# Performance work log

Measured on AMD Instinct MI355X. Metric: run time of the kernel, lower is better.

The kernel has to match this reference:

```python
import jax, jax.numpy as jnp
import numpy as np

HEADS = 8
DIM = 512


def setup_inputs() -> dict:
    key = jax.random.key(0)
    ks = jax.random.split(key, 7)
    B, N, L, C = 2, 64, 32, DIM
    feat1 = jax.random.normal(ks[0], (B, N, L, C), dtype=jnp.float32)
    feat2 = jax.random.normal(ks[1], (B, N, L, C), dtype=jnp.float32)
    s = 1.0 / np.sqrt(C)
    Wq1 = jax.random.normal(ks[2], (C, C), dtype=jnp.float32) * s
    Wk1 = jax.random.normal(ks[3], (C, C), dtype=jnp.float32) * s
    Wq2 = jax.random.normal(ks[4], (C, C), dtype=jnp.float32) * s
    Wk2 = jax.random.normal(ks[5], (C, C), dtype=jnp.float32) * s
    tau = jnp.array(0.3, dtype=jnp.float32)
    return {"feat1": feat1, "feat2": feat2, "Wq1": Wq1, "Wk1": Wk1,
            "Wq2": Wq2, "Wk2": Wk2, "tau": tau}


def _proj_heads(x_flat, W, B, NL, H):
    # nn.Linear(bias=False): y = x @ W.T ; then split heads -> (B, H, NL, hd)
    y = jnp.einsum('btc,dc->btd', x_flat, W)
    return y.reshape(B, NL, H, -1).transpose(0, 2, 1, 3)


def _pooled_scores(Q, Kt, scale, tau, B, H, N, L):
    # scores (B,H,NL,NL) -> softmax -> view (B,H,N,L,N,L) -> amax(-1) -> mean(L) -> mean(H)
    s = jnp.einsum('bhqd,bhkd->bhqk', Q, Kt) * (scale / tau)
    s = jax.nn.softmax(s, axis=-1)
    s = s.reshape(B, H, N, L, N, L)
    s = s.max(axis=-1)          # (B,H,N,L,N)
    s = s.mean(axis=3)          # (B,H,N,N)
    return s.mean(axis=1)       # (B,N,N)


def reference(feat1, feat2, Wq1, Wk1, Wq2, Wk2, tau):
    B, N, L, C = feat1.shape
    H = HEADS
    NL = N * L
    scale = C ** (-0.5)
    f1 = feat1.reshape(B, NL, C)
    f2 = feat2.reshape(B, NL, C)
    Q1 = _proj_heads(f1, Wq1, B, NL, H)
    K1 = _proj_heads(f1, Wk1, B, NL, H)
    Q2 = _proj_heads(f2, Wq2, B, NL, H)
    K2 = _proj_heads(f2, Wk2, B, NL, H)
    c12 = _pooled_scores(Q1, K2, scale, tau, B, H, N, L)
    c21 = _pooled_scores(Q2, K1, scale, tau, B, H, N, L)
    return (c12 + c21) * 0.5
```

## Files before the change

kernel.cpp:

```cpp
#include <hip/hip_runtime.h>
#include <hip/hip_bf16.h>

#define NLQ 2048
#define CDIM 512
#define HD 64
#define NHEADS 8

typedef __attribute__((ext_vector_type(8))) short bf16x8;
typedef __attribute__((ext_vector_type(4))) float f32x4;

#define MFMA(A, B, Cc) __builtin_amdgcn_mfma_f32_16x16x32_bf16(A, B, Cc, 0, 0, 0)

__device__ __forceinline__ short f2bf(float x) {
    __hip_bfloat16 h = __float2bfloat16(x);
    return *reinterpret_cast<short*>(&h);
}

__device__ __forceinline__ float fast_exp2(float x) {
    float r;
    asm("v_exp_f32 %0, %1" : "=v"(r) : "v"(x));
    return r;
}

__device__ __forceinline__ int swz(int row, int colByte) {
    return ((row << 7) + colByte) ^ ((row & 7) << 4);
}

#define QK_ELEMS   8388608
#define X_ELEMS    2097152
#define W_ELEMS    262144
#define PLANE      2097152

__global__ __launch_bounds__(256) void convert_kernel(
    const float* __restrict__ f1, const float* __restrict__ f2,
    const float* __restrict__ Wq1, const float* __restrict__ Wk1,
    const float* __restrict__ Wq2, const float* __restrict__ Wk2,
    const float* __restrict__ tau, short* __restrict__ ws)
{
    short* Xb1 = ws + QK_ELEMS;
    short* Xb2 = Xb1 + X_ELEMS;
    short* Wb  = Xb2 + X_ELEMS;
    float la = 0.044194173824159216f * 1.4426950408889634f / tau[0];

    int bid = blockIdx.x;
    const float* src; short* dst; float a = 1.0f; int idx;
    if (bid < 1024)       { src = f1; dst = Xb1; idx = bid; }
    else if (bid < 2048)  { src = f2; dst = Xb2; idx = bid - 1024; }
    else {
        int wseg = (bid - 2048) >> 7;
        idx = (bid - 2048) & 127;
        src = (wseg == 0) ? Wq1 : (wseg == 1) ? Wk1 : (wseg == 2) ? Wq2 : Wk2;
        dst = Wb + wseg * W_ELEMS;
        a = (wseg == 0 || wseg == 2) ? la : 1.0f;
    }
    int off = idx * 2048 + threadIdx.x * 8;
    float4 x0 = *(const float4*)(src + off);
    float4 x1 = *(const float4*)(src + off + 4);
    bf16x8 v = { f2bf(x0.x * a), f2bf(x0.y * a), f2bf(x0.z * a), f2bf(x0.w * a),
                 f2bf(x1.x * a), f2bf(x1.y * a), f2bf(x1.z * a), f2bf(x1.w * a) };
    *(bf16x8*)(dst + off) = v;
}

__global__ __launch_bounds__(256) void proj_kernel(short* __restrict__ ws)
{
    int bid = blockIdx.x;
    int gx = bid >> 8;
    int mt = (bid >> 3) & 31;
    int nt = bid & 7;

    const short* X   = ws + QK_ELEMS + gx * X_ELEMS;
    const short* Wst = ws + QK_ELEMS + 2 * X_ELEMS + gx * (2 * W_ELEMS);
    short* Yb = ws;

    __shared__ alignas(16) short Alds[2][8192];
    __shared__ alignas(16) short Blds[2][8192];

    int t = threadIdx.x;
    int lane = t & 63;
    int w = t >> 6;
    int wr = w >> 1, wc = w & 1;
    int m0 = mt * 128, d0 = nt * 128;

    int srow = t >> 1;
    int sh = (t & 1) * 32;
    const short* xsrc = X   + (m0 + srow) * CDIM + sh;
    const short* wsrc = Wst + (d0 + srow) * CDIM + sh;

    f32x4 acc[4][4] = {};

    bf16x8 wv0 = *(const bf16x8*)(wsrc);
    bf16x8 wv1 = *(const bf16x8*)(wsrc + 8);
    bf16x8 wv2 = *(const bf16x8*)(wsrc + 16);
    bf16x8 wv3 = *(const bf16x8*)(wsrc + 24);
    bf16x8 xv0 = *(const bf16x8*)(xsrc);
    bf16x8 xv1 = *(const bf16x8*)(xsrc + 8);
    bf16x8 xv2 = *(const bf16x8*)(xsrc + 16);
    bf16x8 xv3 = *(const bf16x8*)(xsrc + 24);
    {
        int b0 = sh * 2;
        *(bf16x8*)((char*)Alds[0] + swz(srow, b0))      = wv0;
        *(bf16x8*)((char*)Alds[0] + swz(srow, b0 + 16)) = wv1;
        *(bf16x8*)((char*)Alds[0] + swz(srow, b0 + 32)) = wv2;
        *(bf16x8*)((char*)Alds[0] + swz(srow, b0 + 48)) = wv3;
        *(bf16x8*)((char*)Blds[0] + swz(srow, b0))      = xv0;
        *(bf16x8*)((char*)Blds[0] + swz(srow, b0 + 16)) = xv1;
        *(bf16x8*)((char*)Blds[0] + swz(srow, b0 + 32)) = xv2;
        *(bf16x8*)((char*)Blds[0] + swz(srow, b0 + 48)) = xv3;
    }
    __syncthreads();

    for (int kc = 0; kc < 8; ++kc) {
        int cur = kc & 1;
        if (kc < 7) {
            const short* xn = xsrc + (kc + 1) * 64;
            const short* wn = wsrc + (kc + 1) * 64;
            wv0 = *(const bf16x8*)(wn);      wv1 = *(const bf16x8*)(wn + 8);
            wv2 = *(const bf16x8*)(wn + 16); wv3 = *(const bf16x8*)(wn + 24);
            xv0 = *(const bf16x8*)(xn);      xv1 = *(const bf16x8*)(xn + 8);
            xv2 = *(const bf16x8*)(xn + 16); xv3 = *(const bf16x8*)(xn + 24);
        }
        int cb = (lane >> 4) << 4;
        bf16x8 bfr[4][2];
        #pragma unroll
        for (int ms = 0; ms < 4; ++ms) {
            int row = (wr << 6) + (ms << 4) + (lane & 15);
            bfr[ms][0] = *(const bf16x8*)((const char*)Blds[cur] + swz(row, cb));
            bfr[ms][1] = *(const bf16x8*)((const char*)Blds[cur] + swz(row, cb + 64));
        }
        #pragma unroll
        for (int ns = 0; ns < 4; ++ns) {
            int arow = (wc << 6) + (ns << 4) + (lane & 15);
            bf16x8 a0 = *(const bf16x8*)((const char*)Alds[cur] + swz(arow, cb));
            bf16x8 a1 = *(const bf16x8*)((const char*)Alds[cur] + swz(arow, cb + 64));
            #pragma unroll
            for (int ms = 0; ms < 4; ++ms) {
                acc[ms][ns] = MFMA(a0, bfr[ms][0], acc[ms][ns]);
                acc[ms][ns] = MFMA(a1, bfr[ms][1], acc[ms][ns]);
            }
        }
        if (kc < 7) {
            int nx = cur ^ 1;
            int b0 = sh * 2;
            *(bf16x8*)((char*)Alds[nx] + swz(srow, b0))      = wv0;
            *(bf16x8*)((char*)Alds[nx] + swz(srow, b0 + 16)) = wv1;
            *(bf16x8*)((char*)Alds[nx] + swz(srow, b0 + 32)) = wv2;
            *(bf16x8*)((char*)Alds[nx] + swz(srow, b0 + 48)) = wv3;
            *(bf16x8*)((char*)Blds[nx] + swz(srow, b0))      = xv0;
            *(bf16x8*)((char*)Blds[nx] + swz(srow, b0 + 16)) = xv1;
            *(bf16x8*)((char*)Blds[nx] + swz(srow, b0 + 32)) = xv2;
            *(bf16x8*)((char*)Blds[nx] + swz(srow, b0 + 48)) = xv3;
        }
        __syncthreads();
    }

    #pragma unroll
    for (int ms = 0; ms < 4; ++ms) {
        int m = m0 + (wr << 6) + (ms << 4) + (lane & 15);
        int bb = m >> 11, tl = m & 2047;
        #pragma unroll
        for (int ns = 0; ns < 4; ++ns) {
            int d = d0 + (wc << 6) + (ns << 4) + ((lane >> 4) << 2);
            int plane = (gx << 1) + (d >> 9);
            int head = (d >> 6) & 7;
            int hd = d & 63;
            short4 v = { f2bf(acc[ms][ns][0]), f2bf(acc[ms][ns][1]),
                         f2bf(acc[ms][ns][2]), f2bf(acc[ms][ns][3]) };
            *(short4*)(Yb + plane * PLANE + ((bb * NHEADS + head) * NLQ + tl) * HD + hd) = v;
        }
    }
}

__global__ __launch_bounds__(256) void attn_kernel(
    const short* __restrict__ qk, float* __restrict__ out)
{
    int bid = blockIdx.x;
    int combo = bid & 31;
    int qt = bid >> 5;
    int h    = combo & 7;
    int pair = (combo >> 3) & 1;
    int b    = combo >> 4;

    const short* Q = qk + (pair ? 2 : 0) * PLANE + (b * NHEADS + h) * NLQ * HD;
    const short* K = qk + (pair ? 1 : 3) * PLANE + (b * NHEADS + h) * NLQ * HD;

    __shared__ float bms[64][65];
    __shared__ float psums[4][64];
    __shared__ float rowinv[64];
    __shared__ float partial[4][64];

    int t = threadIdx.x;
    int lane = t & 63;
    int w = t >> 6;

    bf16x8 qb[4][2];
    #pragma unroll
    for (int qs = 0; qs < 4; ++qs) {
        int row = qt * 64 + (qs << 4) + (lane & 15);
        const short* qp = Q + row * HD + ((lane >> 4) << 3);
        qb[qs][0] = *(const bf16x8*)qp;
        qb[qs][1] = *(const bf16x8*)(qp + 32);
    }

    float ps[4] = {0.f, 0.f, 0.f, 0.f};

    for (int i = 0; i < 8; ++i) {
        int kt = (w << 3) + i;
        int k0 = kt << 6;

        bf16x8 af[4][2];
        #pragma unroll
        for (int ks = 0; ks < 4; ++ks) {
            const short* kp = K + (k0 + (ks << 4) + (lane & 15)) * HD + ((lane >> 4) << 3);
            af[ks][0] = *(const bf16x8*)kp;
            af[ks][1] = *(const bf16x8*)(kp + 32);
        }

        f32x4 acc[4][4] = {};
        #pragma unroll
        for (int ks = 0; ks < 4; ++ks) {
            #pragma unroll
            for (int qs = 0; qs < 4; ++qs) {
                acc[ks][qs] = MFMA(af[ks][0], qb[qs][0], acc[ks][qs]);
                acc[ks][qs] = MFMA(af[ks][1], qb[qs][1], acc[ks][qs]);
            }
        }

        #pragma unroll
        for (int qs = 0; qs < 4; ++qs) {
            float g0 = (fast_exp2(acc[0][qs][0]) + fast_exp2(acc[0][qs][1]))
                     + (fast_exp2(acc[0][qs][2]) + fast_exp2(acc[0][qs][3]));
            float g1 = (fast_exp2(acc[1][qs][0]) + fast_exp2(acc[1][qs][1]))
                     + (fast_exp2(acc[1][qs][2]) + fast_exp2(acc[1][qs][3]));
            float g2 = (fast_exp2(acc[2][qs][0]) + fast_exp2(acc[2][qs][1]))
                     + (fast_exp2(acc[2][qs][2]) + fast_exp2(acc[2][qs][3]));
            float g3 = (fast_exp2(acc[3][qs][0]) + fast_exp2(acc[3][qs][1]))
                     + (fast_exp2(acc[3][qs][2]) + fast_exp2(acc[3][qs][3]));
            ps[qs] += (g0 + g1) + (g2 + g3);

            float a0 = fmaxf(fmaxf(acc[0][qs][0], acc[0][qs][1]), acc[0][qs][2]);
            float a1 = fmaxf(fmaxf(acc[0][qs][3], acc[1][qs][0]), acc[1][qs][1]);
            float bm0 = fmaxf(fmaxf(a0, a1), fmaxf(acc[1][qs][2], acc[1][qs][3]));
            float a2 = fmaxf(fmaxf(acc[2][qs][0], acc[2][qs][1]), acc[2][qs][2]);
            float a3 = fmaxf(fmaxf(acc[2][qs][3], acc[3][qs][0]), acc[3][qs][1]);
            float bm1 = fmaxf(fmaxf(a2, a3), fmaxf(acc[3][qs][2], acc[3][qs][3]));

            bm0 = fmaxf(bm0, __shfl_xor(bm0, 16));
            bm0 = fmaxf(bm0, __shfl_xor(bm0, 32));
            bm1 = fmaxf(bm1, __shfl_xor(bm1, 16));
            bm1 = fmaxf(bm1, __shfl_xor(bm1, 32));
            if (lane < 16) {
                bms[2 * kt][(qs << 4) + lane]     = bm0;
                bms[2 * kt + 1][(qs << 4) + lane] = bm1;
            }
        }
    }

    #pragma unroll
    for (int qs = 0; qs < 4; ++qs) {
        float s = ps[qs];
        s += __shfl_xor(s, 16);
        s += __shfl_xor(s, 32);
        if (lane < 16) psums[w][(qs << 4) + lane] = s;
    }
    __syncthreads();
    if (t < 64) rowinv[t] = 1.0f /
        ((psums[0][t] + psums[1][t]) + (psums[2][t] + psums[3][t]));
    __syncthreads();

    {
        int n2 = t & 63;
        int rg = t >> 6;
        float a = 0.f;
        #pragma unroll
        for (int r = rg * 16; r < rg * 16 + 16; ++r)
            a += fast_exp2(bms[n2][r]) * rowinv[r];
        partial[rg][n2] = a;
    }
    __syncthreads();

    if (t < 128) {
        int n1l = t >> 6, n2 = t & 63;
        float val = (partial[2 * n1l][n2] + partial[2 * n1l + 1][n2]) * (1.0f / 512.0f);
        atomicAdd(&out[(b * 64 + qt * 2 + n1l) * 64 + n2], val);
    }
}

extern "C" void kernel_launch(void* const* d_in, const int* in_sizes, int n_in,
                              void* d_out, int out_size, void* d_ws, size_t ws_size,
                              hipStream_t stream) {
    const float* f1  = (const float*)d_in[0];
    const float* f2  = (const float*)d_in[1];
    const float* Wq1 = (const float*)d_in[2];
    const float* Wk1 = (const float*)d_in[3];
    const float* Wq2 = (const float*)d_in[4];
    const float* Wk2 = (const float*)d_in[5];
    const float* tau = (const float*)d_in[6];
    float* out = (float*)d_out;
    short* ws = (short*)d_ws;

    hipMemsetAsync(d_out, 0, (size_t)out_size * sizeof(float), stream);
    convert_kernel<<<dim3(2560), dim3(256), 0, stream>>>(f1, f2, Wq1, Wk1, Wq2, Wk2, tau, ws);
    proj_kernel<<<dim3(512), dim3(256), 0, stream>>>(ws);
    attn_kernel<<<dim3(1024), dim3(256), 0, stream>>>(ws, out);
}
```

Measured before the change: 134.9 us.

## Prefetch next K tile during score MFMA and interleave exp/max per query subtile

```diff
diff --git a/kernel.cpp b/kernel.cpp
--- a/kernel.cpp
+++ b/kernel.cpp
@@ -10,16 +10,11 @@
 typedef __attribute__((ext_vector_type(4))) float f32x4;
 
 #define MFMA(A, B, Cc) __builtin_amdgcn_mfma_f32_16x16x32_bf16(A, B, Cc, 0, 0, 0)
+#define EXP2(x) __builtin_amdgcn_exp2f(x)
 
 __device__ __forceinline__ short f2bf(float x) {
     __hip_bfloat16 h = __float2bfloat16(x);
     return *reinterpret_cast<short*>(&h);
-}
-
-__device__ __forceinline__ float fast_exp2(float x) {
-    float r;
-    asm("v_exp_f32 %0, %1" : "=v"(r) : "v"(x));
-    return r;
 }
 
 __device__ __forceinline__ int swz(int row, int colByte) {
@@ -201,48 +196,49 @@
         qb[qs][1] = *(const bf16x8*)(qp + 32);
     }
 
+    const short* kp = K + ((w << 9) + (lane & 15)) * HD + ((lane >> 4) << 3);
+
     float ps[4] = {0.f, 0.f, 0.f, 0.f};
 
+    bf16x8 af[4][2];
+    #pragma unroll
+    for (int ks = 0; ks < 4; ++ks) {
+        af[ks][0] = *(const bf16x8*)(kp + ks * 1024);
+        af[ks][1] = *(const bf16x8*)(kp + ks * 1024 + 32);
+    }
+
+    #pragma unroll
     for (int i = 0; i < 8; ++i) {
         int kt = (w << 3) + i;
-        int k0 = kt << 6;
-
-        bf16x8 af[4][2];
-        #pragma unroll
-        for (int ks = 0; ks < 4; ++ks) {
-            const short* kp = K + (k0 + (ks << 4) + (lane & 15)) * HD + ((lane >> 4) << 3);
-            af[ks][0] = *(const bf16x8*)kp;
-            af[ks][1] = *(const bf16x8*)(kp + 32);
-        }
-
-        f32x4 acc[4][4] = {};
-        #pragma unroll
-        for (int ks = 0; ks < 4; ++ks) {
-            #pragma unroll
-            for (int qs = 0; qs < 4; ++qs) {
-                acc[ks][qs] = MFMA(af[ks][0], qb[qs][0], acc[ks][qs]);
-                acc[ks][qs] = MFMA(af[ks][1], qb[qs][1], acc[ks][qs]);
+        #pragma unroll
+        for (int qs = 0; qs < 4; ++qs) {
+            f32x4 c0 = {}, c1 = {}, c2 = {}, c3 = {};
+            c0 = MFMA(af[0][0], qb[qs][0], c0); c0 = MFMA(af[0][1], qb[qs][1], c0);
+            c1 = MFMA(af[1][0], qb[qs][0], c1); c1 = MFMA(af[1][1], qb[qs][1], c1);
+            c2 = MFMA(af[2][0], qb[qs][0], c2); c2 = MFMA(af[2][1], qb[qs][1], c2);
+            c3 = MFMA(af[3][0], qb[qs][0], c3); c3 = MFMA(af[3][1], qb[qs][1], c3);
+
+            if (qs == 3 && i < 7) {
+                const short* kn = kp + (i + 1) * 4096;
+                #pragma unroll
+                for (int ks = 0; ks < 4; ++ks) {
+                    af[ks][0] = *(const bf16x8*)(kn + ks * 1024);
+                    af[ks][1] = *(const bf16x8*)(kn + ks * 1024 + 32);
+                }
             }
-        }
-
-        #pragma unroll
-        for (int qs = 0; qs < 4; ++qs) {
-            float g0 = (fast_exp2(acc[0][qs][0]) + fast_exp2(acc[0][qs][1]))
-                     + (fast_exp2(acc[0][qs][2]) + fast_exp2(acc[0][qs][3]));
-            float g1 = (fast_exp2(acc[1][qs][0]) + fast_exp2(acc[1][qs][1]))
-                     + (fast_exp2(acc[1][qs][2]) + fast_exp2(acc[1][qs][3]));
-            float g2 = (fast_exp2(acc[2][qs][0]) + fast_exp2(acc[2][qs][1]))
-                     + (fast_exp2(acc[2][qs][2]) + fast_exp2(acc[2][qs][3]));
-            float g3 = (fast_exp2(acc[3][qs][0]) + fast_exp2(acc[3][qs][1]))
-                     + (fast_exp2(acc[3][qs][2]) + fast_exp2(acc[3][qs][3]));
+
+            float g0 = (EXP2(c0[0]) + EXP2(c0[1])) + (EXP2(c0[2]) + EXP2(c0[3]));
+            float g1 = (EXP2(c1[0]) + EXP2(c1[1])) + (EXP2(c1[2]) + EXP2(c1[3]));
+            float g2 = (EXP2(c2[0]) + EXP2(c2[1])) + (EXP2(c2[2]) + EXP2(c2[3]));
+            float g3 = (EXP2(c3[0]) + EXP2(c3[1])) + (EXP2(c3[2]) + EXP2(c3[3]));
             ps[qs] += (g0 + g1) + (g2 + g3);
 
-            float a0 = fmaxf(fmaxf(acc[0][qs][0], acc[0][qs][1]), acc[0][qs][2]);
-            float a1 = fmaxf(fmaxf(acc[0][qs][3], acc[1][qs][0]), acc[1][qs][1]);
-            float bm0 = fmaxf(fmaxf(a0, a1), fmaxf(acc[1][qs][2], acc[1][qs][3]));
-            float a2 = fmaxf(fmaxf(acc[2][qs][0], acc[2][qs][1]), acc[2][qs][2]);
-            float a3 = fmaxf(fmaxf(acc[2][qs][3], acc[3][qs][0]), acc[3][qs][1]);
-            float bm1 = fmaxf(fmaxf(a2, a3), fmaxf(acc[3][qs][2], acc[3][qs][3]));
+            float a0 = fmaxf(fmaxf(c0[0], c0[1]), c0[2]);
+            float a1 = fmaxf(fmaxf(c0[3], c1[0]), c1[1]);
+            float bm0 = fmaxf(fmaxf(a0, a1), fmaxf(c1[2], c1[3]));
+            float a2 = fmaxf(fmaxf(c2[0], c2[1]), c2[2]);
+            float a3 = fmaxf(fmaxf(c2[3], c3[0]), c3[1]);
+            float bm1 = fmaxf(fmaxf(a2, a3), fmaxf(c3[2], c3[3]));
 
             bm0 = fmaxf(bm0, __shfl_xor(bm0, 16));
             bm0 = fmaxf(bm0, __shfl_xor(bm0, 32));
@@ -273,7 +269,7 @@
         float a = 0.f;
         #pragma unroll
         for (int r = rg * 16; r < rg * 16 + 16; ++r)
-            a += fast_exp2(bms[n2][r]) * rowinv[r];
+            a += EXP2(bms[n2][r]) * rowinv[r];
         partial[rg][n2] = a;
     }
     __syncthreads();
```

After: 158.2 us. 17.2% more time.
